# Performance work log

Hardware: AMD Instinct MI355X
Metric: run time of the kernel (lower is better)

## Reference

```python
import jax, jax.numpy as jnp
import numpy as np

NUM_CLASSES = 3
DICE_W, FOCAL_W, CONTR_W = 1.0, 1.0, 0.1
GAMMA, ALPHA = 2.0, 0.25
TEMP = 0.1
SCALE_WEIGHTS = (1.0, 0.8, 0.6)
SMOOTH = 1e-5


def setup_inputs() -> dict:
    key = jax.random.key(0)
    ks = jax.random.split(key, 7)
    return {
        "pred_maps": jax.random.normal(ks[0], (2, 3, 128, 128, 128), jnp.float32),
        "target": jax.random.randint(ks[1], (2, 128, 128, 128), 0, 3, jnp.int64),
        "fmap0": jax.random.normal(ks[2], (2, 48, 16, 16, 16), jnp.float32),
        "fmap1": jax.random.normal(ks[3], (2, 48, 8, 8, 8), jnp.float32),
        "fmap2": jax.random.normal(ks[4], (2, 48, 4, 4, 4), jnp.float32),
        "logits": jax.random.normal(ks[5], (2, 3), jnp.float32),
        "labels": jax.random.randint(ks[6], (2, 3), 0, 2, jnp.int32),
    }


def _dice_loss(pred, target):
    p = jax.nn.softmax(pred, axis=1)                      # [B,C,H,W,D]
    t = jnp.where(target == -1, 0, target)
    oh = jax.nn.one_hot(t, NUM_CLASSES, axis=1, dtype=p.dtype)  # [B,C,H,W,D]
    inter = (p * oh).sum((2, 3, 4))                       # [B,C]
    union = p.sum((2, 3, 4)) + oh.sum((2, 3, 4))
    dice = (2.0 * inter + SMOOTH) / (union + SMOOTH)      # [B,C]
    return 1.0 - dice[:, 1:].mean()                       # exclude background


def _focal_loss(logits, labels):
    pt = jax.nn.sigmoid(logits)
    pt = jnp.where(labels == 1, pt, 1.0 - pt)
    return (-ALPHA * (1.0 - pt) ** GAMMA * jnp.log(pt + 1e-6)).mean()


def _pair_loss(E, wa, wb, offdiag, positive):
    # E: [B,N,N] exp(sim/T); wa, wb: [B,N] class indicator weights
    W = wa[:, :, None] * wb[:, None, :]
    if offdiag is not None:
        W = W * offdiag
    cnt = W.sum((1, 2))
    mean = (E * W).sum((1, 2)) / jnp.maximum(cnt, 1.0)
    val = -jnp.log(mean + 1e-6) if positive else jnp.log1p(mean)
    return jnp.where(cnt > 0, val, 0.0)                   # [B]


def _scale_loss(feat, mask):
    B, C = feat.shape[:2]
    f = feat.reshape(B, C, -1)                            # [B,C,N]
    norm = jnp.sqrt((f * f).sum(1, keepdims=True))
    f = f / jnp.maximum(norm, 1e-12)                      # F.normalize(dim=1)
    m = mask.reshape(B, -1)                               # [B,N]
    E = jnp.exp(jnp.einsum('bcn,bcm->bnm', f, f) / TEMP)  # [B,N,N]
    N = m.shape[1]
    off = 1.0 - jnp.eye(N, dtype=f.dtype)
    w0 = (m == 0).astype(f.dtype)
    w1 = (m == 1).astype(f.dtype)
    w2 = (m == 2).astype(f.dtype)
    loss = _pair_loss(E, w1, w1, off, True)               # htx positive
    loss += _pair_loss(E, w2, w2, off, True)              # mh positive
    loss += _pair_loss(E, w1, w2, None, False)            # htx vs mh
    loss += _pair_loss(E, w0, w1, None, False)            # bg vs htx
    loss += _pair_loss(E, w0, w2, None, False)            # bg vs mh
    return loss.mean()                                    # batch_loss / B


def _contrastive_loss(fmaps, target):
    H = target.shape[1]
    total = 0.0
    for feat, w in zip(fmaps, SCALE_WEIGHTS):
        s = H // feat.shape[2]                            # exact nearest-downsample stride
        mask = target[:, ::s, ::s, ::s]
        total += w * _scale_loss(feat, mask)
    return total


def reference(pred_maps, target, fmap0, fmap1, fmap2, logits, labels):
    dice = _dice_loss(pred_maps, target)
    focal = _focal_loss(logits, labels)
    contr = _contrastive_loss((fmap0, fmap1, fmap2), target)
    total = DICE_W * dice + FOCAL_W * focal + CONTR_W * contr
    return (total, dice, focal, contr)
```

## Files before the change

kernel.cpp:

```cpp
#include <hip/hip_runtime.h>
#include <math.h>

#define VOX (128*128*128)
#define NCH 48
#define SCL 3.16227766f

typedef _Float16 half8 __attribute__((ext_vector_type(8)));
typedef float floatx4 __attribute__((ext_vector_type(4)));

__device__ __forceinline__ float waveSum(float v) {
#pragma unroll
    for (int off = 32; off > 0; off >>= 1) v += __shfl_down(v, off, 64);
    return v;
}


__device__ __forceinline__ int elem_class(const int* __restrict__ target,
                                          int scale, int b, int n) {
    const int d = (scale == 0) ? 16 : (scale == 1) ? 8 : 4;
    const int s = 128 / d;
    int i3 = n % d, i2 = (n / d) % d, i1 = n / (d * d);
    return target[(size_t)b * VOX + (size_t)(i1 * s) * 16384 + (i2 * s) * 128 + (i3 * s)];
}

__global__ __launch_bounds__(256) void count_kernel(const int* __restrict__ target,
                                                    int* __restrict__ count_stage,
                                                    int* __restrict__ cls0,
                                                    int* __restrict__ cls1,
                                                    int* __restrict__ cls2) {
    const int scale = blockIdx.y, b = blockIdx.z, z = scale * 2 + b, bx = blockIdx.x;
    const int N    = (scale == 0) ? 4096 : (scale == 1) ? 512 : 64;
    const int Npad = (scale == 0) ? 4096 : (scale == 1) ? 512 : 128;
    const int n = bx * 256 + threadIdx.x;
    int myK = -1;
    if (n < N)          myK = elem_class(target, scale, b, n);
    else if (n < Npad)  myK = 3;
    if (n < Npad)
        (((scale == 0) ? cls0 : (scale == 1) ? cls1 : cls2) + b * Npad)[n] = myK;

    __shared__ int wc[4][4];
    const int lane = threadIdx.x & 63, w = threadIdx.x >> 6;
#pragma unroll
    for (int k = 0; k < 4; k++) {
        unsigned long long mb = __ballot(myK == k);
        if (lane == 0) wc[w][k] = (int)__popcll(mb);
    }
    __syncthreads();
    if (threadIdx.x < 4)
        count_stage[(z * 16 + bx) * 4 + threadIdx.x] =
            wc[0][threadIdx.x] + wc[1][threadIdx.x] + wc[2][threadIdx.x] + wc[3][threadIdx.x];
}

__global__ __launch_bounds__(256) void norm_scatter(const float* __restrict__ f0in,
                                                    const float* __restrict__ f1in,
                                                    const float* __restrict__ f2in,
                                                    const int* __restrict__ cls0,
                                                    const int* __restrict__ cls1,
                                                    const int* __restrict__ cls2,
                                                    _Float16* __restrict__ Fh0,
                                                    _Float16* __restrict__ Fh1,
                                                    _Float16* __restrict__ Fh2,
                                                    const int* __restrict__ count_stage,
                                                    int* __restrict__ cnt) {
    const int scale = blockIdx.y, b = blockIdx.z, z = scale * 2 + b, bx = blockIdx.x;
    const int N    = (scale == 0) ? 4096 : (scale == 1) ? 512 : 64;
    const int Npad = (scale == 0) ? 4096 : (scale == 1) ? 512 : 128;
    if (bx * 256 >= Npad) return;
    const int tid = threadIdx.x, lane = tid & 63, w = tid >> 6;
    const int n = bx * 256 + tid;

    __shared__ int cs[64];
    __shared__ int wcls[4][4];
    if (tid < 64) cs[tid] = count_stage[z * 64 + tid];

    int myK = -1;
    if (n < Npad)
        myK = (((scale == 0) ? cls0 : (scale == 1) ? cls1 : cls2) + b * Npad)[n];

    const unsigned long long below = (1ull << lane) - 1ull;
    int laneRank = 0;
#pragma unroll
    for (int k = 0; k < 4; k++) {
        unsigned long long mb = __ballot(myK == k);
        if (lane == 0) wcls[w][k] = (int)__popcll(mb);
        if (myK == k) laneRank = (int)__popcll(mb & below);
    }
    __syncthreads();

    int total[4];
#pragma unroll
    for (int k = 0; k < 4; k++) {
        int s = 0;
        for (int r = 0; r < 16; r++) s += cs[r * 4 + k];
        total[k] = s;
    }
    if (bx == 0 && tid < 4) cnt[z * 4 + tid] = total[tid];
    if (myK < 0) return;

    int dest = laneRank;
    for (int k = 0; k < myK; k++) dest += total[k];
    for (int r = 0; r < bx; r++) dest += cs[r * 4 + myK];
    for (int ww = 0; ww < w; ww++) dest += wcls[ww][myK];

    float v[NCH];
    float inv = 0.0f;
    if (n < N) {
        const float* fi = ((scale == 0) ? f0in : (scale == 1) ? f1in : f2in)
                          + (size_t)b * NCH * N + n;
        float ss = 0.0f;
#pragma unroll
        for (int c = 0; c < NCH; c++) { v[c] = fi[(size_t)c * N]; ss += v[c] * v[c]; }
        inv = SCL / fmaxf(sqrtf(ss), 1e-12f);
    } else {
#pragma unroll
        for (int c = 0; c < NCH; c++) v[c] = 0.0f;
    }
    _Float16* fo = ((scale == 0) ? Fh0 : (scale == 1) ? Fh1 : Fh2)
                   + (size_t)b * Npad * 64 + (size_t)dest * 64;
#pragma unroll
    for (int g = 0; g < 8; g++) {
        half8 h;
#pragma unroll
        for (int e = 0; e < 8; e++) {
            int c = g * 8 + e;
            h[e] = (c < NCH) ? (_Float16)(v[c] * inv) : (_Float16)0.0f;
        }
        *(half8*)(fo + g * 8) = h;
    }
}

__global__ __launch_bounds__(256) void dice_pair(const float* __restrict__ pred,
                                                 const int* __restrict__ target,
                                                 const _Float16* __restrict__ Fh0,
                                                 const _Float16* __restrict__ Fh1,
                                                 const _Float16* __restrict__ Fh2,
                                                 const int* __restrict__ cnt,
                                                 float* __restrict__ dice_stage,
                                                 float* __restrict__ pair_stage) {
    const int bid = blockIdx.x;
    const int tid = threadIdx.x, lane = tid & 63, w = tid >> 6;
    __shared__ float red[4][6];

    if (bid >= 550) {
        const int local = bid - 550;
        const int b = local >> 9, bx = local & 511;
        const float4* p0 = (const float4*)(pred + (size_t)b * 3 * VOX);
        const float4* p1 = (const float4*)(pred + (size_t)b * 3 * VOX + VOX);
        const float4* p2 = (const float4*)(pred + (size_t)b * 3 * VOX + 2 * VOX);
        const int4*   tg = (const int4*)(target + (size_t)b * VOX);

        float vals[6] = {0, 0, 0, 0, 0, 0};
        const int V4 = VOX / 4;
        for (int v = bx * 256 + tid; v < V4; v += 512 * 256) {
            float4 a = p0[v], bq = p1[v], cq = p2[v];
            int4 t = tg[v];
            float xs[4][3] = {{a.x, bq.x, cq.x}, {a.y, bq.y, cq.y},
                              {a.z, bq.z, cq.z}, {a.w, bq.w, cq.w}};
            int ts[4] = {t.x, t.y, t.z, t.w};
#pragma unroll
            for (int e = 0; e < 4; e++) {
                float e0 = __expf(xs[e][0]), e1 = __expf(xs[e][1]), e2 = __expf(xs[e][2]);
                float inv = 1.0f / (e0 + e1 + e2);
                float q1 = e1 * inv, q2 = e2 * inv;
                vals[2] += q1;
                vals[3] += q2;
                int tt = ts[e];
                vals[0] += (tt == 1) ? q1 : 0.0f;
                vals[1] += (tt == 2) ? q2 : 0.0f;
                vals[4] += (tt == 1) ? 1.0f : 0.0f;
                vals[5] += (tt == 2) ? 1.0f : 0.0f;
            }
        }
#pragma unroll
        for (int k = 0; k < 6; k++) {
            float s = waveSum(vals[k]);
            if (lane == 0) red[w][k] = s;
        }
        __syncthreads();
        if (tid < 6) {
            float s = red[0][tid] + red[1][tid] + red[2][tid] + red[3][tid];
            dice_stage[(size_t)local * 8 + tid] = s;
        }
        return;
    }

    int z, t0, nt, tstep;
    if (bid < 528)      { z = bid / 264; t0 = bid % 264; nt = 2; tstep = 264; }
    else if (bid < 548) { int i = bid - 528; z = 2 + i / 10; t0 = i % 10; nt = 1; tstep = 0; }
    else                { z = 4 + (bid - 548); t0 = 0; nt = 1; tstep = 0; }

    const int scale = z >> 1, b = z & 1;
    const int Npad = (scale == 0) ? 4096 : (scale == 1) ? 512 : 128;
    const _Float16* F = ((scale == 0) ? Fh0 : (scale == 1) ? Fh1 : Fh2)
                        + (size_t)b * Npad * 64;
    const int B1 = cnt[z * 4 + 0];
    const int B2 = B1 + cnt[z * 4 + 1];
    const int B3 = B2 + cnt[z * 4 + 2];

    const int wi = w >> 1, wj = w & 1;
    const int m = lane & 15, q = lane >> 4;

    float s[5] = {0, 0, 0, 0, 0};

    for (int it = 0; it < nt; it++) {
        int t = t0 + it * tstep;
        int by = (int)((sqrtf(8.0f * (float)t + 1.0f) - 1.0f) * 0.5f);
        while ((by + 1) * (by + 2) / 2 <= t) by++;
        while (by * (by + 1) / 2 > t) by--;
        int bx = t - by * (by + 1) / 2;

        const int ib = bx * 128 + wi * 64, jb = by * 128 + wj * 64;

        const bool diag = (ib == jb);
        const bool belowq = (ib > jb);
        int ciL = (ib >= B1) + (ib >= B2) + (ib >= B3);
        int ciH = (ib + 63 >= B1) + (ib + 63 >= B2) + (ib + 63 >= B3);
        int cjL = (jb >= B1) + (jb >= B2) + (jb >= B3);
        int cjH = (jb + 63 >= B1) + (jb + 63 >= B2) + (jb + 63 >= B3);
        const bool pure = (ciL == ciH) && (cjL == cjH) && !diag;
        int bucket = -1;
        float mult = 1.0f;
        if (pure) {
            int ci = ciL, cj = cjL;
            if (ci == 1 && cj == 1) { bucket = 0; mult = 2.0f; }
            else if (ci == 2 && cj == 2) { bucket = 1; mult = 2.0f; }
            else if (ci == 1 && cj == 2) bucket = 2;
            else if (ci == 0 && cj == 1) bucket = 3;
            else if (ci == 0 && cj == 2) bucket = 4;
        }
        if (belowq || (pure && bucket < 0)) continue;

        const _Float16* Ai = F + (size_t)(ib + m) * 64 + q * 8;
        const _Float16* Bj = F + (size_t)(jb + m) * 64 + q * 8;

        floatx4 acc_[4][4] = {};
#pragma unroll
        for (int k = 0; k < 2; k++) {
            half8 aF[4], bF[4];
#pragma unroll
            for (int t4 = 0; t4 < 4; t4++) {
                aF[t4] = *(const half8*)(Ai + t4 * 16 * 64 + k * 32);
                bF[t4] = *(const half8*)(Bj + t4 * 16 * 64 + k * 32);
            }
#pragma unroll
            for (int ti = 0; ti < 4; ti++)
#pragma unroll
                for (int tj = 0; tj < 4; tj++)
                    acc_[ti][tj] = __builtin_amdgcn_mfma_f32_16x16x32_f16(
                        aF[ti], bF[tj], acc_[ti][tj], 0, 0, 0);
        }

        if (pure) {
            float ps[4] = {0, 0, 0, 0};
#pragma unroll
            for (int ti = 0; ti < 4; ti++)
#pragma unroll
                for (int tj = 0; tj < 4; tj++)
#pragma unroll
                    for (int r = 0; r < 4; r++)
                        ps[r] += __expf(acc_[ti][tj][r]);
            s[bucket] += ((ps[0] + ps[1]) + (ps[2] + ps[3])) * mult;
        } else {
#pragma unroll
            for (int ti = 0; ti < 4; ti++) {
#pragma unroll
                for (int tj = 0; tj < 4; tj++) {
#pragma unroll
                    for (int r = 0; r < 4; r++) {
                        int gi = ib + ti * 16 + q * 4 + r;
                        int gj = jb + tj * 16 + m;
                        float e = __expf(acc_[ti][tj][r]);
                        bool ok = !diag || (gi < gj);
                        int ci = (gi >= B1) + (gi >= B2) + (gi >= B3);
                        int cj = (gj >= B1) + (gj >= B2) + (gj >= B3);
                        s[0] += (ok && ci == 1 && cj == 1) ? e + e : 0.0f;
                        s[1] += (ok && ci == 2 && cj == 2) ? e + e : 0.0f;
                        s[2] += (ok && ci == 1 && cj == 2) ? e : 0.0f;
                        s[3] += (ok && ci == 0 && cj == 1) ? e : 0.0f;
                        s[4] += (ok && ci == 0 && cj == 2) ? e : 0.0f;
                    }
                }
            }
        }
    }

#pragma unroll
    for (int k = 0; k < 5; k++) {
        float r = waveSum(s[k]);
        if (lane == 0) red[w][k] = r;
    }
    __syncthreads();
    if (tid < 5) {
        float r = red[0][tid] + red[1][tid] + red[2][tid] + red[3][tid];
        pair_stage[(size_t)bid * 8 + tid] = r;
    }
}

__global__ __launch_bounds__(512) void reduce_finalize(const float* __restrict__ dice_stage,
                                                       const int* __restrict__ cnt,
                                                       const float* __restrict__ pair_stage,
                                                       const float* __restrict__ logits,
                                                       const int* __restrict__ labels,
                                                       float* __restrict__ out) {
    __shared__ float D[2][6], S[6][5];
    const int tid = threadIdx.x, w = tid >> 6, lane = tid & 63;

    if (w < 2) {
        float v[6] = {0, 0, 0, 0, 0, 0};
#pragma unroll
        for (int i = 0; i < 8; i++) {
            const float* row = dice_stage + (size_t)(w * 512 + i * 64 + lane) * 8;
#pragma unroll
            for (int k = 0; k < 6; k++) v[k] += row[k];
        }
#pragma unroll
        for (int k = 0; k < 6; k++) {
            float r = waveSum(v[k]);
            if (lane == 0) D[w][k] = r;
        }
    } else {
        int z = w - 2;
        int start = (z == 0) ? 0 : (z == 1) ? 264 : (z == 2) ? 528
                    : (z == 3) ? 538 : (z == 4) ? 548 : 549;
        int n = (z < 2) ? 264 : (z < 4) ? 10 : 1;
        float v[5] = {0, 0, 0, 0, 0};
        for (int i = lane; i < n; i += 64) {
            const float* row = pair_stage + (size_t)(start + i) * 8;
#pragma unroll
            for (int k = 0; k < 5; k++) v[k] += row[k];
        }
#pragma unroll
        for (int k = 0; k < 5; k++) {
            float r = waveSum(v[k]);
            if (lane == 0) S[z][k] = r;
        }
    }
    __syncthreads();
    if (tid != 0) return;

    float dsum = 0.0f;
    for (int b = 0; b < 2; b++)
        for (int c = 0; c < 2; c++)
            dsum += (2.0f * D[b][c] + 1e-5f) / (D[b][2 + c] + D[b][4 + c] + 1e-5f);
    float dice = 1.0f - dsum * 0.25f;

    float fsum = 0.0f;
    for (int i = 0; i < 6; i++) {
        float x = logits[i];
        float pt = 1.0f / (1.0f + __expf(-x));
        if (labels[i] != 1) pt = 1.0f - pt;
        fsum += -0.25f * (1.0f - pt) * (1.0f - pt) * logf(pt + 1e-6f);
    }
    float focal = fsum * (1.0f / 6.0f);

    const float sw[3] = {1.0f, 0.8f, 0.6f};
    float contr = 0.0f;
    for (int sc = 0; sc < 3; sc++) {
        float bsum = 0.0f;
        for (int b = 0; b < 2; b++) {
            int z = sc * 2 + b;
            float S11 = S[z][0], S22 = S[z][1], S12 = S[z][2],
                  S01 = S[z][3], S02 = S[z][4];
            float c0 = (float)cnt[z * 4 + 0], c1 = (float)cnt[z * 4 + 1],
                  c2 = (float)cnt[z * 4 + 2];
            float l = 0.0f, c, mean;
            c = c1 * c1 - c1; mean = S11 / fmaxf(c, 1.0f);
            l += (c > 0.0f) ? -logf(mean + 1e-6f) : 0.0f;
            c = c2 * c2 - c2; mean = S22 / fmaxf(c, 1.0f);
            l += (c > 0.0f) ? -logf(mean + 1e-6f) : 0.0f;
            c = c1 * c2; mean = S12 / fmaxf(c, 1.0f);
            l += (c > 0.0f) ? log1pf(mean) : 0.0f;
            c = c0 * c1; mean = S01 / fmaxf(c, 1.0f);
            l += (c > 0.0f) ? log1pf(mean) : 0.0f;
            c = c0 * c2; mean = S02 / fmaxf(c, 1.0f);
            l += (c > 0.0f) ? log1pf(mean) : 0.0f;
            bsum += l;
        }
        contr += sw[sc] * bsum * 0.5f;
    }
    float total = dice + focal + 0.1f * contr;
    out[0] = total;
    out[1] = dice;
    out[2] = focal;
    out[3] = contr;
}

extern "C" void kernel_launch(void* const* d_in, const int* in_sizes, int n_in,
                              void* d_out, int out_size, void* d_ws, size_t ws_size,
                              hipStream_t stream) {
    const float* pred   = (const float*)d_in[0];
    const int*   target = (const int*)d_in[1];
    const float* f0     = (const float*)d_in[2];
    const float* f1     = (const float*)d_in[3];
    const float* f2     = (const float*)d_in[4];
    const float* logits = (const float*)d_in[5];
    const int*   labels = (const int*)d_in[6];
    float* out = (float*)d_out;

    char* ws = (char*)d_ws;
    int*   cnt         = (int*)ws;
    int*   count_stage = (int*)(ws + 1024);
    float* dice_stage  = (float*)(ws + 4096);
    float* pair_stage  = (float*)(ws + 36864);
    int*   cls0 = (int*)(ws + 73728);
    int*   cls1 = (int*)(ws + 106496);
    int*   cls2 = (int*)(ws + 110592);
    _Float16* Fh0 = (_Float16*)(ws + 131072);
    _Float16* Fh1 = (_Float16*)(ws + 1179648);
    _Float16* Fh2 = (_Float16*)(ws + 1310720);

    count_kernel<<<dim3(16, 3, 2), dim3(256), 0, stream>>>(target, count_stage,
                                                           cls0, cls1, cls2);
    norm_scatter<<<dim3(16, 3, 2), dim3(256), 0, stream>>>(f0, f1, f2,
                                                           cls0, cls1, cls2,
                                                           Fh0, Fh1, Fh2,
                                                           count_stage, cnt);
    dice_pair<<<dim3(1574), dim3(256), 0, stream>>>(pred, target, Fh0, Fh1, Fh2,
                                                    cnt, dice_stage, pair_stage);
    reduce_finalize<<<dim3(1), dim3(512), 0, stream>>>(dice_stage, cnt, pair_stage,
                                                       logits, labels, out);
}
```

Measured before the change: 128.8 us.

## Spread dice reduction across the small count and scatter kernels

The dice softmax/one-hot reduction over the large prediction volume is split into four strips. Two strips now run in extra blocks of the count kernel, one in the scatter kernel, and one stays in dice_pair. Before this, the count and scatter launches used only 96 blocks and left most of the GPU idle, so this fills those launches with bandwidth-bound work. The final reducer now sums three regions of dice partials, and the workspace offsets are shifted to make room for them.

```diff
diff --git a/kernel.cpp b/kernel.cpp
--- a/kernel.cpp
+++ b/kernel.cpp
@@ -23,37 +23,91 @@
     return target[(size_t)b * VOX + (size_t)(i1 * s) * 16384 + (i2 * s) * 128 + (i3 * s)];
 }
 
-__global__ __launch_bounds__(256) void count_kernel(const int* __restrict__ target,
-                                                    int* __restrict__ count_stage,
-                                                    int* __restrict__ cls0,
-                                                    int* __restrict__ cls1,
-                                                    int* __restrict__ cls2) {
-    const int scale = blockIdx.y, b = blockIdx.z, z = scale * 2 + b, bx = blockIdx.x;
-    const int N    = (scale == 0) ? 4096 : (scale == 1) ? 512 : 64;
-    const int Npad = (scale == 0) ? 4096 : (scale == 1) ? 512 : 128;
-    const int n = bx * 256 + threadIdx.x;
-    int myK = -1;
-    if (n < N)          myK = elem_class(target, scale, b, n);
-    else if (n < Npad)  myK = 3;
-    if (n < Npad)
-        (((scale == 0) ? cls0 : (scale == 1) ? cls1 : cls2) + b * Npad)[n] = myK;
-
-    __shared__ int wc[4][4];
-    const int lane = threadIdx.x & 63, w = threadIdx.x >> 6;
-#pragma unroll
-    for (int k = 0; k < 4; k++) {
-        unsigned long long mb = __ballot(myK == k);
-        if (lane == 0) wc[w][k] = (int)__popcll(mb);
+__device__ __forceinline__ void dice_strip(const float4* __restrict__ predq,
+                                           const int4* __restrict__ tgq,
+                                           int b, int v, float* vals) {
+    const size_t base = (size_t)b * 1572864 + v;
+    float4 a = predq[base], bq = predq[base + 524288], cq = predq[base + 1048576];
+    int4 t = tgq[(size_t)b * 524288 + v];
+    float xs[4][3] = {{a.x, bq.x, cq.x}, {a.y, bq.y, cq.y},
+                      {a.z, bq.z, cq.z}, {a.w, bq.w, cq.w}};
+    int ts[4] = {t.x, t.y, t.z, t.w};
+#pragma unroll
+    for (int e = 0; e < 4; e++) {
+        float e0 = __expf(xs[e][0]), e1 = __expf(xs[e][1]), e2 = __expf(xs[e][2]);
+        float inv = 1.0f / (e0 + e1 + e2);
+        float q1 = e1 * inv, q2 = e2 * inv;
+        vals[2] += q1;
+        vals[3] += q2;
+        int tt = ts[e];
+        vals[0] += (tt == 1) ? q1 : 0.0f;
+        vals[1] += (tt == 2) ? q2 : 0.0f;
+        vals[4] += (tt == 1) ? 1.0f : 0.0f;
+        vals[5] += (tt == 2) ? 1.0f : 0.0f;
+    }
+}
+
+__device__ __forceinline__ void dice_reduce_store(float* __restrict__ row,
+                                                  float vals[6], int tid) {
+    __shared__ float red[4][6];
+    const int lane = tid & 63, w = tid >> 6;
+#pragma unroll
+    for (int k = 0; k < 6; k++) {
+        float s = waveSum(vals[k]);
+        if (lane == 0) red[w][k] = s;
     }
     __syncthreads();
-    if (threadIdx.x < 4)
-        count_stage[(z * 16 + bx) * 4 + threadIdx.x] =
-            wc[0][threadIdx.x] + wc[1][threadIdx.x] + wc[2][threadIdx.x] + wc[3][threadIdx.x];
-}
-
-__global__ __launch_bounds__(256) void norm_scatter(const float* __restrict__ f0in,
+    if (tid < 6)
+        row[tid] = red[0][tid] + red[1][tid] + red[2][tid] + red[3][tid];
+}
+
+__global__ __launch_bounds__(256) void count_dice(const int* __restrict__ target,
+                                                  const float* __restrict__ pred,
+                                                  int* __restrict__ count_stage,
+                                                  int* __restrict__ cls0,
+                                                  int* __restrict__ cls1,
+                                                  int* __restrict__ cls2,
+                                                  float* __restrict__ dice_stage) {
+    const int bid = blockIdx.x, tid = threadIdx.x;
+    if (bid < 96) {
+        const int b = bid / 48, scale = (bid % 48) / 16, bx = bid % 16;
+        const int z = scale * 2 + b;
+        const int N    = (scale == 0) ? 4096 : (scale == 1) ? 512 : 64;
+        const int Npad = (scale == 0) ? 4096 : (scale == 1) ? 512 : 128;
+        const int n = bx * 256 + tid;
+        int myK = -1;
+        if (n < N)          myK = elem_class(target, scale, b, n);
+        else if (n < Npad)  myK = 3;
+        if (n < Npad)
+            (((scale == 0) ? cls0 : (scale == 1) ? cls1 : cls2) + b * Npad)[n] = myK;
+
+        __shared__ int wc[4][4];
+        const int lane = tid & 63, w = tid >> 6;
+#pragma unroll
+        for (int k = 0; k < 4; k++) {
+            unsigned long long mb = __ballot(myK == k);
+            if (lane == 0) wc[w][k] = (int)__popcll(mb);
+        }
+        __syncthreads();
+        if (tid < 4)
+            count_stage[(z * 16 + bx) * 4 + tid] =
+                wc[0][tid] + wc[1][tid] + wc[2][tid] + wc[3][tid];
+        return;
+    }
+    const int local = bid - 96;
+    const int b = local >> 9, bx = local & 511;
+    const int v0 = bx * 256 + tid;
+    float vals[6] = {0, 0, 0, 0, 0, 0};
+    dice_strip((const float4*)pred, (const int4*)target, b, v0, vals);
+    dice_strip((const float4*)pred, (const int4*)target, b, v0 + 131072, vals);
+    dice_reduce_store(dice_stage + (size_t)local * 8, vals, tid);
+}
+
+__global__ __launch_bounds__(256) void scatter_dice(const float* __restrict__ f0in,
                                                     const float* __restrict__ f1in,
                                                     const float* __restrict__ f2in,
+                                                    const int* __restrict__ target,
+                                                    const float* __restrict__ pred,
                                                     const int* __restrict__ cls0,
                                                     const int* __restrict__ cls1,
                                                     const int* __restrict__ cls2,
@@ -61,72 +115,84 @@
                                                     _Float16* __restrict__ Fh1,
                                                     _Float16* __restrict__ Fh2,
                                                     const int* __restrict__ count_stage,
-                                                    int* __restrict__ cnt) {
-    const int scale = blockIdx.y, b = blockIdx.z, z = scale * 2 + b, bx = blockIdx.x;
-    const int N    = (scale == 0) ? 4096 : (scale == 1) ? 512 : 64;
-    const int Npad = (scale == 0) ? 4096 : (scale == 1) ? 512 : 128;
-    if (bx * 256 >= Npad) return;
-    const int tid = threadIdx.x, lane = tid & 63, w = tid >> 6;
-    const int n = bx * 256 + tid;
-
-    __shared__ int cs[64];
-    __shared__ int wcls[4][4];
-    if (tid < 64) cs[tid] = count_stage[z * 64 + tid];
-
-    int myK = -1;
-    if (n < Npad)
-        myK = (((scale == 0) ? cls0 : (scale == 1) ? cls1 : cls2) + b * Npad)[n];
-
-    const unsigned long long below = (1ull << lane) - 1ull;
-    int laneRank = 0;
-#pragma unroll
-    for (int k = 0; k < 4; k++) {
-        unsigned long long mb = __ballot(myK == k);
-        if (lane == 0) wcls[w][k] = (int)__popcll(mb);
-        if (myK == k) laneRank = (int)__popcll(mb & below);
-    }
-    __syncthreads();
-
-    int total[4];
-#pragma unroll
-    for (int k = 0; k < 4; k++) {
-        int s = 0;
-        for (int r = 0; r < 16; r++) s += cs[r * 4 + k];
-        total[k] = s;
-    }
-    if (bx == 0 && tid < 4) cnt[z * 4 + tid] = total[tid];
-    if (myK < 0) return;
-
-    int dest = laneRank;
-    for (int k = 0; k < myK; k++) dest += total[k];
-    for (int r = 0; r < bx; r++) dest += cs[r * 4 + myK];
-    for (int ww = 0; ww < w; ww++) dest += wcls[ww][myK];
-
-    float v[NCH];
-    float inv = 0.0f;
-    if (n < N) {
-        const float* fi = ((scale == 0) ? f0in : (scale == 1) ? f1in : f2in)
-                          + (size_t)b * NCH * N + n;
-        float ss = 0.0f;
-#pragma unroll
-        for (int c = 0; c < NCH; c++) { v[c] = fi[(size_t)c * N]; ss += v[c] * v[c]; }
-        inv = SCL / fmaxf(sqrtf(ss), 1e-12f);
-    } else {
-#pragma unroll
-        for (int c = 0; c < NCH; c++) v[c] = 0.0f;
-    }
-    _Float16* fo = ((scale == 0) ? Fh0 : (scale == 1) ? Fh1 : Fh2)
-                   + (size_t)b * Npad * 64 + (size_t)dest * 64;
-#pragma unroll
-    for (int g = 0; g < 8; g++) {
-        half8 h;
-#pragma unroll
-        for (int e = 0; e < 8; e++) {
-            int c = g * 8 + e;
-            h[e] = (c < NCH) ? (_Float16)(v[c] * inv) : (_Float16)0.0f;
-        }
-        *(half8*)(fo + g * 8) = h;
-    }
+                                                    int* __restrict__ cnt,
+                                                    float* __restrict__ dice_stage) {
+    const int bid = blockIdx.x, tid = threadIdx.x;
+    if (bid < 96) {
+        const int b = bid / 48, scale = (bid % 48) / 16, bx = bid % 16;
+        const int z = scale * 2 + b;
+        const int N    = (scale == 0) ? 4096 : (scale == 1) ? 512 : 64;
+        const int Npad = (scale == 0) ? 4096 : (scale == 1) ? 512 : 128;
+        if (bx * 256 >= Npad) return;
+        const int lane = tid & 63, w = tid >> 6;
+        const int n = bx * 256 + tid;
+
+        __shared__ int cs[64];
+        __shared__ int wcls[4][4];
+        if (tid < 64) cs[tid] = count_stage[z * 64 + tid];
+
+        int myK = -1;
+        if (n < Npad)
+            myK = (((scale == 0) ? cls0 : (scale == 1) ? cls1 : cls2) + b * Npad)[n];
+
+        const unsigned long long below = (1ull << lane) - 1ull;
+        int laneRank = 0;
+#pragma unroll
+        for (int k = 0; k < 4; k++) {
+            unsigned long long mb = __ballot(myK == k);
+            if (lane == 0) wcls[w][k] = (int)__popcll(mb);
+            if (myK == k) laneRank = (int)__popcll(mb & below);
+        }
+        __syncthreads();
+
+        int total[4];
+#pragma unroll
+        for (int k = 0; k < 4; k++) {
+            int s = 0;
+            for (int r = 0; r < 16; r++) s += cs[r * 4 + k];
+            total[k] = s;
+        }
+        if (bx == 0 && tid < 4) cnt[z * 4 + tid] = total[tid];
+        if (myK < 0) return;
+
+        int dest = laneRank;
+        for (int k = 0; k < myK; k++) dest += total[k];
+        for (int r = 0; r < bx; r++) dest += cs[r * 4 + myK];
+        for (int ww = 0; ww < w; ww++) dest += wcls[ww][myK];
+
+        float v[NCH];
+        float inv = 0.0f;
+        if (n < N) {
+            const float* fi = ((scale == 0) ? f0in : (scale == 1) ? f1in : f2in)
+                              + (size_t)b * NCH * N + n;
+            float ss = 0.0f;
+#pragma unroll
+            for (int c = 0; c < NCH; c++) { v[c] = fi[(size_t)c * N]; ss += v[c] * v[c]; }
+            inv = SCL / fmaxf(sqrtf(ss), 1e-12f);
+        } else {
+#pragma unroll
+            for (int c = 0; c < NCH; c++) v[c] = 0.0f;
+        }
+        _Float16* fo = ((scale == 0) ? Fh0 : (scale == 1) ? Fh1 : Fh2)
+                       + (size_t)b * Npad * 64 + (size_t)dest * 64;
+#pragma unroll
+        for (int g = 0; g < 8; g++) {
+            half8 h;
+#pragma unroll
+            for (int e = 0; e < 8; e++) {
+                int c = g * 8 + e;
+                h[e] = (c < NCH) ? (_Float16)(v[c] * inv) : (_Float16)0.0f;
+            }
+            *(half8*)(fo + g * 8) = h;
+        }
+        return;
+    }
+    const int local = bid - 96;
+    const int b = local >> 9, bx = local & 511;
+    float vals[6] = {0, 0, 0, 0, 0, 0};
+    dice_strip((const float4*)pred, (const int4*)target, b,
+               bx * 256 + tid + 262144, vals);
+    dice_reduce_store(dice_stage + (size_t)(1024 + local) * 8, vals, tid);
 }
 
 __global__ __launch_bounds__(256) void dice_pair(const float* __restrict__ pred,
@@ -139,48 +205,14 @@
                                                  float* __restrict__ pair_stage) {
     const int bid = blockIdx.x;
     const int tid = threadIdx.x, lane = tid & 63, w = tid >> 6;
-    __shared__ float red[4][6];
 
     if (bid >= 550) {
         const int local = bid - 550;
         const int b = local >> 9, bx = local & 511;
-        const float4* p0 = (const float4*)(pred + (size_t)b * 3 * VOX);
-        const float4* p1 = (const float4*)(pred + (size_t)b * 3 * VOX + VOX);
-        const float4* p2 = (const float4*)(pred + (size_t)b * 3 * VOX + 2 * VOX);
-        const int4*   tg = (const int4*)(target + (size_t)b * VOX);
-
         float vals[6] = {0, 0, 0, 0, 0, 0};
-        const int V4 = VOX / 4;
-        for (int v = bx * 256 + tid; v < V4; v += 512 * 256) {
-            float4 a = p0[v], bq = p1[v], cq = p2[v];
-            int4 t = tg[v];
-            float xs[4][3] = {{a.x, bq.x, cq.x}, {a.y, bq.y, cq.y},
-                              {a.z, bq.z, cq.z}, {a.w, bq.w, cq.w}};
-            int ts[4] = {t.x, t.y, t.z, t.w};
-#pragma unroll
-            for (int e = 0; e < 4; e++) {
-                float e0 = __expf(xs[e][0]), e1 = __expf(xs[e][1]), e2 = __expf(xs[e][2]);
-                float inv = 1.0f / (e0 + e1 + e2);
-                float q1 = e1 * inv, q2 = e2 * inv;
-                vals[2] += q1;
-                vals[3] += q2;
-                int tt = ts[e];
-                vals[0] += (tt == 1) ? q1 : 0.0f;
-                vals[1] += (tt == 2) ? q2 : 0.0f;
-                vals[4] += (tt == 1) ? 1.0f : 0.0f;
-                vals[5] += (tt == 2) ? 1.0f : 0.0f;
-            }
-        }
-#pragma unroll
-        for (int k = 0; k < 6; k++) {
-            float s = waveSum(vals[k]);
-            if (lane == 0) red[w][k] = s;
-        }
-        __syncthreads();
-        if (tid < 6) {
-            float s = red[0][tid] + red[1][tid] + red[2][tid] + red[3][tid];
-            dice_stage[(size_t)local * 8 + tid] = s;
-        }
+        dice_strip((const float4*)pred, (const int4*)target, b,
+                   bx * 256 + tid + 393216, vals);
+        dice_reduce_store(dice_stage + (size_t)(2048 + local) * 8, vals, tid);
         return;
     }
 
@@ -284,6 +316,7 @@
         }
     }
 
+    __shared__ float red[4][5];
 #pragma unroll
     for (int k = 0; k < 5; k++) {
         float r = waveSum(s[k]);
@@ -307,9 +340,9 @@
 
     if (w < 2) {
         float v[6] = {0, 0, 0, 0, 0, 0};
-#pragma unroll
-        for (int i = 0; i < 8; i++) {
-            const float* row = dice_stage + (size_t)(w * 512 + i * 64 + lane) * 8;
+        for (int i = lane; i < 1536; i += 64) {
+            int reg = i >> 9, bx = i & 511;
+            const float* row = dice_stage + (size_t)(reg * 1024 + w * 512 + bx) * 8;
 #pragma unroll
             for (int k = 0; k < 6; k++) v[k] += row[k];
         }
@@ -401,20 +434,20 @@
     int*   cnt         = (int*)ws;
     int*   count_stage = (int*)(ws + 1024);
     float* dice_stage  = (float*)(ws + 4096);
-    float* pair_stage  = (float*)(ws + 36864);
-    int*   cls0 = (int*)(ws + 73728);
-    int*   cls1 = (int*)(ws + 106496);
-    int*   cls2 = (int*)(ws + 110592);
-    _Float16* Fh0 = (_Float16*)(ws + 131072);
-    _Float16* Fh1 = (_Float16*)(ws + 1179648);
-    _Float16* Fh2 = (_Float16*)(ws + 1310720);
-
-    count_kernel<<<dim3(16, 3, 2), dim3(256), 0, stream>>>(target, count_stage,
-                                                           cls0, cls1, cls2);
-    norm_scatter<<<dim3(16, 3, 2), dim3(256), 0, stream>>>(f0, f1, f2,
-                                                           cls0, cls1, cls2,
-                                                           Fh0, Fh1, Fh2,
-                                                           count_stage, cnt);
+    float* pair_stage  = (float*)(ws + 102400);
+    int*   cls0 = (int*)(ws + 120832);
+    int*   cls1 = (int*)(ws + 153600);
+    int*   cls2 = (int*)(ws + 157696);
+    _Float16* Fh0 = (_Float16*)(ws + 163840);
+    _Float16* Fh1 = (_Float16*)(ws + 1212416);
+    _Float16* Fh2 = (_Float16*)(ws + 1343488);
+
+    count_dice<<<dim3(1120), dim3(256), 0, stream>>>(target, pred, count_stage,
+                                                     cls0, cls1, cls2, dice_stage);
+    scatter_dice<<<dim3(1120), dim3(256), 0, stream>>>(f0, f1, f2, target, pred,
+                                                       cls0, cls1, cls2,
+                                                       Fh0, Fh1, Fh2,
+                                                       count_stage, cnt, dice_stage);
     dice_pair<<<dim3(1574), dim3(256), 0, stream>>>(pred, target, Fh0, Fh1, Fh2,
                                                     cnt, dice_stage, pair_stage);
     reduce_finalize<<<dim3(1), dim3(512), 0, stream>>>(dice_stage, cnt, pair_stage,
```

Result: slower. 141.0 us (+9.4%).
